# Kernel optimization log

Measured on AMD Instinct MI355X. Metric: run time of the kernel, lower is better.

## Reference

```python
import jax, jax.numpy as jnp
import numpy as np
import math

INPUT_DIM = 1024
DIM_K = 1024
DIM_V = 1024
B, N = 4, 2048

def setup_inputs() -> dict:
    key = jax.random.key(0)
    ks = jax.random.split(key, 7)
    s = 1.0 / math.sqrt(INPUT_DIM)
    return {
        'x':  jax.random.normal(ks[0], (B, N, INPUT_DIM), dtype=jnp.float32),
        'Wq': jax.random.uniform(ks[1], (DIM_K, INPUT_DIM), jnp.float32, -s, s),
        'bq': jax.random.uniform(ks[2], (DIM_K,), jnp.float32, -s, s),
        'Wk': jax.random.uniform(ks[3], (DIM_K, INPUT_DIM), jnp.float32, -s, s),
        'bk': jax.random.uniform(ks[4], (DIM_K,), jnp.float32, -s, s),
        'Wv': jax.random.uniform(ks[5], (DIM_V, INPUT_DIM), jnp.float32, -s, s),
        'bv': jax.random.uniform(ks[6], (DIM_V,), jnp.float32, -s, s),
    }

def reference(x, Wq, bq, Wk, bk, Wv, bv):
    norm_fact = 1.0 / math.sqrt(DIM_K)
    # torch Linear: y = x @ W.T + b
    Q = jnp.einsum('bnd,kd->bnk', x, Wq) + bq  # [B,N,dim_k]
    K = jnp.einsum('bnd,kd->bnk', x, Wk) + bk  # [B,N,dim_k]
    V = jnp.einsum('bnd,vd->bnv', x, Wv) + bv  # [B,N,dim_v]
    scores = jnp.einsum('bqk,bnk->bqn', Q, K)  # [B,N,N]
    # NOTE: original code applies softmax FIRST, then scales by norm_fact
    atten = jax.nn.softmax(scores, axis=-1) * norm_fact
    return jnp.einsum('bqn,bnv->bqv', atten, V)  # [B,N,dim_v]
```

## Files before the change

kernel.cpp:

```cpp
#include <hip/hip_runtime.h>


typedef _Float16 hfx8 __attribute__((ext_vector_type(8)));
typedef _Float16 hfx4 __attribute__((ext_vector_type(4)));
typedef float fx4 __attribute__((ext_vector_type(4)));

__device__ __forceinline__ void load_lds16(const void* g, void* l) {
    __builtin_amdgcn_global_load_lds(
        (const __attribute__((address_space(1))) void*)g,
        (__attribute__((address_space(3))) void*)l, 16, 0, 0);
}

template <int N> __device__ __forceinline__ void vmwait() {
    if constexpr (N == 8) asm volatile("s_waitcnt vmcnt(8)" ::: "memory");
    else if constexpr (N == 6) asm volatile("s_waitcnt vmcnt(6)" ::: "memory");
    else asm volatile("s_waitcnt vmcnt(0)" ::: "memory");
}

__device__ __forceinline__ void xcd_remap(int& x, int& y, int& z) {
    const int gx = gridDim.x, gy = gridDim.y;
    const int lin = blockIdx.x + gx * (blockIdx.y + gy * blockIdx.z);
    const int cpx = (gx * gy * gridDim.z) >> 3;
    const int w = (lin & 7) * cpx + (lin >> 3);
    x = w % gx;
    y = (w / gx) % gy;
    z = w / (gx * gy);
}

__global__ __launch_bounds__(256) void convx_kernel(
    const float4* __restrict__ in, _Float16* __restrict__ out)
{
    const int i = blockIdx.x * 256 + threadIdx.x;
    float4 v = in[i];
    hfx4 h;
    h[0] = (_Float16)v.x; h[1] = (_Float16)v.y;
    h[2] = (_Float16)v.z; h[3] = (_Float16)v.w;
    *(hfx4*)&out[(long)i * 4] = h;
}

__global__ __launch_bounds__(256) void convw3_kernel(
    const float4* __restrict__ w0, const float4* __restrict__ w1, const float4* __restrict__ w2,
    _Float16* __restrict__ o0, _Float16* __restrict__ o1, _Float16* __restrict__ o2)
{
    const int wsel = blockIdx.x >> 10;
    const float4* in = wsel == 0 ? w0 : (wsel == 1 ? w1 : w2);
    _Float16* out = wsel == 0 ? o0 : (wsel == 1 ? o1 : o2);
    const int i = (blockIdx.x & 1023) * 256 + threadIdx.x;
    float4 v = in[i];
    hfx4 h;
    h[0] = (_Float16)v.x; h[1] = (_Float16)v.y;
    h[2] = (_Float16)v.z; h[3] = (_Float16)v.w;
    *(hfx4*)&out[(long)i * 4] = h;
}

template <int OMODE>
__global__ __launch_bounds__(256, 2) void gemm2(
    const _Float16* __restrict__ A,
    const _Float16* __restrict__ Bq, const _Float16* __restrict__ Bk, const _Float16* __restrict__ Bv,
    const float* __restrict__ bq, const float* __restrict__ bk, const float* __restrict__ bv,
    float* __restrict__ outF, _Float16* __restrict__ oQ, _Float16* __restrict__ oK, _Float16* __restrict__ oV,
    int K, int lda, int ldb, int ldc, float alpha,
    long sAz, long sBz, long sCz)
{
    constexpr int BM = 128, BN = 128, BK = 64;
    constexpr int LPT = 8;

    __shared__ __attribute__((aligned(16))) _Float16 lds[2][(BM + BN) * BK];

    int bx, by, z;
    xcd_remap(bx, by, z);

    A += (long)z * sAz;
    const _Float16* B = (OMODE == 1) ? (z == 0 ? Bq : (z == 1 ? Bk : Bv))
                                     : Bq + (long)z * sBz;

    const int tid = threadIdx.x;
    const int lane = tid & 63;
    const int wv = tid >> 6;
    const int wr = wv >> 1, wc = wv & 1;
    const int lr = lane & 15, lk = lane >> 4;

    const long m0 = (long)by * BM;
    const long n0 = (long)bx * BN;

    fx4 acc[4][4] = {};

    auto STAGE = [&](int kt, int b) {
#pragma unroll
        for (int i = 0; i < LPT; ++i) {
            const int c = i * 256 + tid;
            if (i < 4) {
                const int row = c >> 3, slot = c & 7;
                load_lds16(A + (m0 + row) * (long)lda + kt + ((slot ^ (row & 7)) << 3),
                           &lds[b][c * 8]);
            } else {
                const int c2 = c - 1024;
                const int row = c2 >> 3, slot = c2 & 7;
                load_lds16(B + (n0 + row) * (long)ldb + kt + ((slot ^ (row & 7)) << 3),
                           &lds[b][BM * BK + c2 * 8]);
            }
        }
    };

    const int NT = K / BK;
    STAGE(0, 0);
    STAGE(BK, 1);
    vmwait<8>();
    __builtin_amdgcn_s_barrier();
    __builtin_amdgcn_sched_barrier(0);

    const int rA0 = wr * 64 + lr;
    const int rB0 = wc * 64 + lr;
    const int eA = (rA0 & 7) << 3;
    const int eB = (rB0 & 7) << 3;

    for (int t = 0; t < NT; ++t) {
        const _Float16* LA = &lds[t & 1][0];
        const _Float16* LB = LA + BM * BK;

        hfx8 bfr[4][2];
#pragma unroll
        for (int nf = 0; nf < 4; ++nf)
#pragma unroll
            for (int ks = 0; ks < 2; ++ks)
                bfr[nf][ks] = *(const hfx8*)&LB[(rB0 + nf * 16) * BK + ((ks * 32 + lk * 8) ^ eB)];

#pragma unroll
        for (int q = 0; q < 4; ++q) {
            hfx8 afr[2];
#pragma unroll
            for (int ks = 0; ks < 2; ++ks)
                afr[ks] = *(const hfx8*)&LA[(rA0 + q * 16) * BK + ((ks * 32 + lk * 8) ^ eA)];
            __builtin_amdgcn_s_setprio(1);
#pragma unroll
            for (int nf = 0; nf < 4; ++nf)
#pragma unroll
                for (int ks = 0; ks < 2; ++ks)
                    acc[q][nf] = __builtin_amdgcn_mfma_f32_16x16x32_f16(
                        afr[ks], bfr[nf][ks], acc[q][nf], 0, 0, 0);
            __builtin_amdgcn_s_setprio(0);
        }

        __builtin_amdgcn_s_barrier();
        if (t + 2 < NT) {
            STAGE((t + 2) * BK, t & 1);
            vmwait<8>();
        } else {
            vmwait<0>();
        }
        __builtin_amdgcn_s_barrier();
        __builtin_amdgcn_sched_barrier(0);
    }

#pragma unroll
    for (int mf = 0; mf < 4; ++mf) {
#pragma unroll
        for (int nf = 0; nf < 4; ++nf) {
            const long row0 = m0 + wr * 64 + mf * 16 + lk * 4;
            const long col = n0 + wc * 64 + nf * 16 + lr;
            if constexpr (OMODE == 0) {
                float* oz = outF + (long)z * sCz;
#pragma unroll
                for (int j = 0; j < 4; ++j)
                    oz[(row0 + j) * (long)ldc + col] = alpha * acc[mf][nf][j];
            } else {
                if (z == 0) {
                    const float bb = bq[col];
#pragma unroll
                    for (int j = 0; j < 4; ++j)
                        oQ[(row0 + j) * 1024 + col] = (_Float16)(acc[mf][nf][j] + bb);
                } else if (z == 1) {
                    const float bb = bk[col];
#pragma unroll
                    for (int j = 0; j < 4; ++j)
                        oK[(row0 + j) * 1024 + col] = (_Float16)(acc[mf][nf][j] + bb);
                } else {
                    const float bb = bv[col];
                    hfx4 pk;
#pragma unroll
                    for (int j = 0; j < 4; ++j) pk[j] = (_Float16)(acc[mf][nf][j] + bb);
                    *(hfx4*)&oV[((row0 >> 11) * 1024 + col) * 2048 + (row0 & 2047)] = pk;
                }
            }
        }
    }
}

__global__ __launch_bounds__(256) void softmax_kernel(float* __restrict__ S)
{
    const long row = blockIdx.x;
    float* r = S + row * 2048;
    const int t = threadIdx.x;

    float4 v0 = *(const float4*)&r[t * 4];
    float4 v1 = *(const float4*)&r[1024 + t * 4];
    float v[8] = {v0.x, v0.y, v0.z, v0.w, v1.x, v1.y, v1.z, v1.w};

    float mx = v[0];
#pragma unroll
    for (int j = 1; j < 8; ++j) mx = fmaxf(mx, v[j]);
#pragma unroll
    for (int o = 32; o; o >>= 1) mx = fmaxf(mx, __shfl_xor(mx, o, 64));

    __shared__ float redm[4];
    __shared__ float reds[4];
    const int w = t >> 6;
    if ((t & 63) == 0) redm[w] = mx;
    __syncthreads();
    mx = fmaxf(fmaxf(redm[0], redm[1]), fmaxf(redm[2], redm[3]));

    float e[8];
    float s = 0.f;
#pragma unroll
    for (int j = 0; j < 8; ++j) {
        e[j] = __expf(v[j] - mx);
        s += e[j];
    }
#pragma unroll
    for (int o = 32; o; o >>= 1) s += __shfl_xor(s, o, 64);
    if ((t & 63) == 0) reds[w] = s;
    __syncthreads();
    s = reds[0] + reds[1] + reds[2] + reds[3];

    const float inv = 1.0f / s;
    hfx4 p0, p1;
#pragma unroll
    for (int j = 0; j < 4; ++j) {
        p0[j] = (_Float16)(e[j] * inv);
        p1[j] = (_Float16)(e[4 + j] * inv);
    }
    _Float16* pr = (_Float16*)r;
    *(hfx4*)&pr[t * 4] = p0;
    *(hfx4*)&pr[1024 + t * 4] = p1;
}

extern "C" void kernel_launch(void* const* d_in, const int* in_sizes, int n_in,
                              void* d_out, int out_size, void* d_ws, size_t ws_size,
                              hipStream_t stream)
{
    const float* x  = (const float*)d_in[0];
    const float* Wq = (const float*)d_in[1];
    const float* bq = (const float*)d_in[2];
    const float* Wk = (const float*)d_in[3];
    const float* bk = (const float*)d_in[4];
    const float* Wv = (const float*)d_in[5];
    const float* bv = (const float*)d_in[6];
    float* out = (float*)d_out;

    _Float16* xs  = (_Float16*)d_ws;
    _Float16* Wqh = xs + 8192ull * 1024;
    _Float16* Wkh = Wqh + 1024ull * 1024;
    _Float16* Wvh = Wkh + 1024ull * 1024;
    _Float16* Qp  = Wvh + 1024ull * 1024;
    _Float16* Ks  = Qp + 8192ull * 1024;
    _Float16* Vt  = Ks + 8192ull * 1024;
    float* S      = (float*)(Vt + 4ull * 1024 * 2048);

    dim3 blk(256);

    convx_kernel<<<8192, blk, 0, stream>>>((const float4*)x, xs);
    convw3_kernel<<<3072, blk, 0, stream>>>(
        (const float4*)Wq, (const float4*)Wk, (const float4*)Wv, Wqh, Wkh, Wvh);

    gemm2<1><<<dim3(8, 64, 3), blk, 0, stream>>>(
        xs, Wqh, Wkh, Wvh, bq, bk, bv,
        nullptr, Qp, Ks, Vt,
        1024, 1024, 1024, 0, 1.0f, 0L, 0L, 0L);

    gemm2<0><<<dim3(16, 16, 4), blk, 0, stream>>>(
        Qp, Ks, nullptr, nullptr, nullptr, nullptr, nullptr,
        S, nullptr, nullptr, nullptr,
        1024, 1024, 1024, 2048, 1.0f,
        2097152L, 2097152L, 4194304L);

    softmax_kernel<<<2048 * 4, blk, 0, stream>>>(S);

    gemm2<0><<<dim3(8, 16, 4), blk, 0, stream>>>(
        (const _Float16*)S, Vt, nullptr, nullptr, nullptr, nullptr, nullptr,
        out, nullptr, nullptr, nullptr,
        2048, 4096, 2048, 1024, 0.03125f,
        8388608L, 2097152L, 2097152L);
}
```

Baseline: 178.5 us.

## Use 256x256-tile 8-wave GEMM with staged quarter prefetch for projections and QK^T

```diff
diff --git a/kernel.cpp b/kernel.cpp
--- a/kernel.cpp
+++ b/kernel.cpp
@@ -54,7 +54,7 @@
 }
 
 template <int OMODE>
-__global__ __launch_bounds__(256, 2) void gemm2(
+__global__ __launch_bounds__(512, 1) void gemm8p(
     const _Float16* __restrict__ A,
     const _Float16* __restrict__ Bq, const _Float16* __restrict__ Bk, const _Float16* __restrict__ Bv,
     const float* __restrict__ bq, const float* __restrict__ bk, const float* __restrict__ bv,
@@ -62,10 +62,8 @@
     int K, int lda, int ldb, int ldc, float alpha,
     long sAz, long sBz, long sCz)
 {
-    constexpr int BM = 128, BN = 128, BK = 64;
-    constexpr int LPT = 8;
-
-    __shared__ __attribute__((aligned(16))) _Float16 lds[2][(BM + BN) * BK];
+    constexpr int BK = 64;
+    __shared__ __attribute__((aligned(16))) _Float16 lds[2][32768];
 
     int bx, by, z;
     xcd_remap(bx, by, z);
@@ -73,6 +71,140 @@
     A += (long)z * sAz;
     const _Float16* B = (OMODE == 1) ? (z == 0 ? Bq : (z == 1 ? Bk : Bv))
                                      : Bq + (long)z * sBz;
+
+    const int tid = threadIdx.x;
+    const int lane = tid & 63;
+    const int wv = tid >> 6;
+    const int wr = wv >> 2, wc = wv & 3;
+    const int lr = lane & 15, lk = lane >> 4;
+
+    const long m0 = (long)by * 256;
+    const long n0 = (long)bx * 256;
+
+    fx4 acc[4][2][4] = {};
+
+    auto SH = [&](int kt, int b, int part, int h) {
+#pragma unroll
+        for (int i = 0; i < 2; ++i) {
+            const int g = i * 512 + tid;
+            const int row = h * 128 + (g >> 3);
+            const int slot = g & 7;
+            const _Float16* src = part ? (B + (n0 + row) * (long)ldb)
+                                       : (A + (m0 + row) * (long)lda);
+            load_lds16(src + kt + ((slot ^ (row & 7)) << 3),
+                       &lds[b][part * 16384 + row * 64 + slot * 8]);
+        }
+    };
+
+    const int NT = K / BK;
+    SH(0, 0, 1, 0); SH(0, 0, 1, 1); SH(0, 0, 0, 0); SH(0, 0, 0, 1);
+    SH(BK, 1, 1, 0); SH(BK, 1, 1, 1); SH(BK, 1, 0, 0);
+    vmwait<6>();
+    __builtin_amdgcn_s_barrier();
+
+    const int e = (lr & 7) << 3;
+
+    for (int t = 0; t < NT; ++t) {
+        const int b = t & 1;
+        const _Float16* LA = &lds[b][0];
+        const _Float16* LB = &lds[b][16384];
+
+        hfx8 bfr[4][2];
+#pragma unroll
+        for (int q = 0; q < 4; ++q) {
+            if (q == 0) {
+#pragma unroll
+                for (int nf = 0; nf < 4; ++nf)
+#pragma unroll
+                    for (int ks = 0; ks < 2; ++ks)
+                        bfr[nf][ks] = *(const hfx8*)&LB[(wc * 64 + nf * 16 + lr) * 64 + ((ks * 32 + lk * 8) ^ e)];
+            }
+            hfx8 afr[2][2];
+#pragma unroll
+            for (int j = 0; j < 2; ++j)
+#pragma unroll
+                for (int ks = 0; ks < 2; ++ks)
+                    afr[j][ks] = *(const hfx8*)&LA[(q * 64 + wr * 32 + j * 16 + lr) * 64 + ((ks * 32 + lk * 8) ^ e)];
+
+            if (q == 0)      { if (t + 1 < NT) SH((t + 1) * BK, b ^ 1, 0, 1); }
+            else if (q == 1) { if (t + 2 < NT) SH((t + 2) * BK, b, 1, 0); }
+            else if (q == 2) { if (t + 2 < NT) SH((t + 2) * BK, b, 1, 1); }
+            else             { if (t + 2 < NT) SH((t + 2) * BK, b, 0, 0); }
+
+            __builtin_amdgcn_s_barrier();
+            asm volatile("s_waitcnt lgkmcnt(0)" ::: "memory");
+            __builtin_amdgcn_sched_barrier(0);
+            __builtin_amdgcn_s_setprio(1);
+#pragma unroll
+            for (int j = 0; j < 2; ++j)
+#pragma unroll
+                for (int nf = 0; nf < 4; ++nf)
+#pragma unroll
+                    for (int ks = 0; ks < 2; ++ks)
+                        acc[q][j][nf] = __builtin_amdgcn_mfma_f32_16x16x32_f16(
+                            afr[j][ks], bfr[nf][ks], acc[q][j][nf], 0, 0, 0);
+            __builtin_amdgcn_s_setprio(0);
+            if (q == 3) {
+                if (t + 2 < NT) vmwait<6>();
+                else if (t + 1 < NT) vmwait<0>();
+            }
+            __builtin_amdgcn_s_barrier();
+        }
+    }
+
+#pragma unroll
+    for (int q = 0; q < 4; ++q) {
+#pragma unroll
+        for (int j = 0; j < 2; ++j) {
+#pragma unroll
+            for (int nf = 0; nf < 4; ++nf) {
+                const long row0 = m0 + q * 64 + wr * 32 + j * 16 + lk * 4;
+                const long col = n0 + wc * 64 + nf * 16 + lr;
+                if constexpr (OMODE == 0) {
+                    float* oz = outF + (long)z * sCz;
+#pragma unroll
+                    for (int jj = 0; jj < 4; ++jj)
+                        oz[(row0 + jj) * (long)ldc + col] = alpha * acc[q][j][nf][jj];
+                } else {
+                    if (z == 0) {
+                        const float bb = bq[col];
+#pragma unroll
+                        for (int jj = 0; jj < 4; ++jj)
+                            oQ[(row0 + jj) * 1024 + col] = (_Float16)(acc[q][j][nf][jj] + bb);
+                    } else if (z == 1) {
+                        const float bb = bk[col];
+#pragma unroll
+                        for (int jj = 0; jj < 4; ++jj)
+                            oK[(row0 + jj) * 1024 + col] = (_Float16)(acc[q][j][nf][jj] + bb);
+                    } else {
+                        const float bb = bv[col];
+                        hfx4 pk;
+#pragma unroll
+                        for (int jj = 0; jj < 4; ++jj) pk[jj] = (_Float16)(acc[q][j][nf][jj] + bb);
+                        *(hfx4*)&oV[((row0 >> 11) * 1024 + col) * 2048 + (row0 & 2047)] = pk;
+                    }
+                }
+            }
+        }
+    }
+}
+
+__global__ __launch_bounds__(256, 2) void gemm2(
+    const _Float16* __restrict__ A, const _Float16* __restrict__ B,
+    float* __restrict__ outF,
+    int K, int lda, int ldb, int ldc, float alpha,
+    long sAz, long sBz, long sCz)
+{
+    constexpr int BM = 128, BN = 128, BK = 64;
+    constexpr int LPT = 8;
+
+    __shared__ __attribute__((aligned(16))) _Float16 lds[2][(BM + BN) * BK];
+
+    int bx, by, z;
+    xcd_remap(bx, by, z);
+
+    A += (long)z * sAz;
+    B += (long)z * sBz;
 
     const int tid = threadIdx.x;
     const int lane = tid & 63;
@@ -158,30 +290,10 @@
         for (int nf = 0; nf < 4; ++nf) {
             const long row0 = m0 + wr * 64 + mf * 16 + lk * 4;
             const long col = n0 + wc * 64 + nf * 16 + lr;
-            if constexpr (OMODE == 0) {
-                float* oz = outF + (long)z * sCz;
-#pragma unroll
-                for (int j = 0; j < 4; ++j)
-                    oz[(row0 + j) * (long)ldc + col] = alpha * acc[mf][nf][j];
-            } else {
-                if (z == 0) {
-                    const float bb = bq[col];
-#pragma unroll
-                    for (int j = 0; j < 4; ++j)
-                        oQ[(row0 + j) * 1024 + col] = (_Float16)(acc[mf][nf][j] + bb);
-                } else if (z == 1) {
-                    const float bb = bk[col];
-#pragma unroll
-                    for (int j = 0; j < 4; ++j)
-                        oK[(row0 + j) * 1024 + col] = (_Float16)(acc[mf][nf][j] + bb);
-                } else {
-                    const float bb = bv[col];
-                    hfx4 pk;
-#pragma unroll
-                    for (int j = 0; j < 4; ++j) pk[j] = (_Float16)(acc[mf][nf][j] + bb);
-                    *(hfx4*)&oV[((row0 >> 11) * 1024 + col) * 2048 + (row0 & 2047)] = pk;
-                }
-            }
+            float* oz = outF + (long)z * sCz;
+#pragma unroll
+            for (int j = 0; j < 4; ++j)
+                oz[(row0 + j) * (long)ldc + col] = alpha * acc[mf][nf][j];
         }
     }
 }
@@ -262,12 +374,12 @@
     convw3_kernel<<<3072, blk, 0, stream>>>(
         (const float4*)Wq, (const float4*)Wk, (const float4*)Wv, Wqh, Wkh, Wvh);
 
-    gemm2<1><<<dim3(8, 64, 3), blk, 0, stream>>>(
+    gemm8p<1><<<dim3(4, 32, 3), 512, 0, stream>>>(
         xs, Wqh, Wkh, Wvh, bq, bk, bv,
         nullptr, Qp, Ks, Vt,
         1024, 1024, 1024, 0, 1.0f, 0L, 0L, 0L);
 
-    gemm2<0><<<dim3(16, 16, 4), blk, 0, stream>>>(
+    gemm8p<0><<<dim3(8, 8, 4), 512, 0, stream>>>(
         Qp, Ks, nullptr, nullptr, nullptr, nullptr, nullptr,
         S, nullptr, nullptr, nullptr,
         1024, 1024, 1024, 2048, 1.0f,
@@ -275,9 +387,8 @@
 
     softmax_kernel<<<2048 * 4, blk, 0, stream>>>(S);
 
-    gemm2<0><<<dim3(8, 16, 4), blk, 0, stream>>>(
-        (const _Float16*)S, Vt, nullptr, nullptr, nullptr, nullptr, nullptr,
-        out, nullptr, nullptr, nullptr,
+    gemm2<<<dim3(8, 16, 4), blk, 0, stream>>>(
+        (const _Float16*)S, Vt, out,
         2048, 4096, 2048, 1024, 0.03125f,
         8388608L, 2097152L, 2097152L);
 }
```

After: 185.7 us. 4.0% more time.

## Fold Q/K projections into a precomputed Wq^T·Wk matrix for attention scores

Applied to the files above, without the earlier changes.

```diff
diff --git a/kernel.cpp b/kernel.cpp
--- a/kernel.cpp
+++ b/kernel.cpp
@@ -13,7 +13,6 @@
 
 template <int N> __device__ __forceinline__ void vmwait() {
     if constexpr (N == 8) asm volatile("s_waitcnt vmcnt(8)" ::: "memory");
-    else if constexpr (N == 6) asm volatile("s_waitcnt vmcnt(6)" ::: "memory");
     else asm volatile("s_waitcnt vmcnt(0)" ::: "memory");
 }
 
@@ -27,38 +26,83 @@
     z = w / (gx * gy);
 }
 
-__global__ __launch_bounds__(256) void convx_kernel(
-    const float4* __restrict__ in, _Float16* __restrict__ out)
-{
-    const int i = blockIdx.x * 256 + threadIdx.x;
-    float4 v = in[i];
-    hfx4 h;
-    h[0] = (_Float16)v.x; h[1] = (_Float16)v.y;
-    h[2] = (_Float16)v.z; h[3] = (_Float16)v.w;
-    *(hfx4*)&out[(long)i * 4] = h;
-}
-
-__global__ __launch_bounds__(256) void convw3_kernel(
-    const float4* __restrict__ w0, const float4* __restrict__ w1, const float4* __restrict__ w2,
-    _Float16* __restrict__ o0, _Float16* __restrict__ o1, _Float16* __restrict__ o2)
-{
-    const int wsel = blockIdx.x >> 10;
-    const float4* in = wsel == 0 ? w0 : (wsel == 1 ? w1 : w2);
-    _Float16* out = wsel == 0 ? o0 : (wsel == 1 ? o1 : o2);
-    const int i = (blockIdx.x & 1023) * 256 + threadIdx.x;
-    float4 v = in[i];
-    hfx4 h;
-    h[0] = (_Float16)v.x; h[1] = (_Float16)v.y;
-    h[2] = (_Float16)v.z; h[3] = (_Float16)v.w;
-    *(hfx4*)&out[(long)i * 4] = h;
+__global__ __launch_bounds__(256) void transpose_w_kernel(
+    const float* __restrict__ Wq, const float* __restrict__ Wk,
+    _Float16* __restrict__ WqT, _Float16* __restrict__ WkT)
+{
+    const float* src = blockIdx.z ? Wk : Wq;
+    _Float16* dst = blockIdx.z ? WkT : WqT;
+    const int d0 = blockIdx.x * 64;
+    const int k0 = blockIdx.y * 64;
+    __shared__ float t[64][65];
+    const int tid = threadIdx.x;
+#pragma unroll
+    for (int i = 0; i < 4; ++i) {
+        const int r = i * 16 + (tid >> 4);
+        const int c = (tid & 15) * 4;
+        const float4 v = *(const float4*)&src[(long)(k0 + r) * 1024 + d0 + c];
+        t[r][c] = v.x; t[r][c + 1] = v.y; t[r][c + 2] = v.z; t[r][c + 3] = v.w;
+    }
+    __syncthreads();
+#pragma unroll
+    for (int i = 0; i < 2; ++i) {
+        const int d = i * 32 + (tid >> 3);
+        const int k = (tid & 7) * 8;
+        hfx8 h;
+#pragma unroll
+        for (int j = 0; j < 8; ++j) h[j] = (_Float16)t[k + j][d];
+        *(hfx8*)&dst[(long)(d0 + d) * 1024 + k0 + k] = h;
+    }
+}
+
+__global__ __launch_bounds__(256) void w2_kernel(
+    const float* __restrict__ bq, const float* __restrict__ Wk, float* __restrict__ w2)
+{
+    const int d = blockIdx.x * 256 + threadIdx.x;
+    float a = 0.f;
+    for (int k = 0; k < 1024; ++k)
+        a = fmaf(bq[k], Wk[(long)k * 1024 + d], a);
+    w2[d] = a;
+}
+
+__global__ __launch_bounds__(256) void conv_all_kernel(
+    const float4* __restrict__ x, _Float16* __restrict__ xs,
+    const float4* __restrict__ wv, _Float16* __restrict__ wvh,
+    const float* __restrict__ w2, float* __restrict__ v)
+{
+    const int b = blockIdx.x;
+    const int tid = threadIdx.x;
+    if (b < 8192) {
+        const long i = (long)b * 256 + tid;
+        const float4 xv = x[i];
+        hfx4 h;
+        h[0] = (_Float16)xv.x; h[1] = (_Float16)xv.y;
+        h[2] = (_Float16)xv.z; h[3] = (_Float16)xv.w;
+        *(hfx4*)&xs[i * 4] = h;
+        const float4 wval = *(const float4*)&w2[tid * 4];
+        float dot = xv.x * wval.x + xv.y * wval.y + xv.z * wval.z + xv.w * wval.w;
+#pragma unroll
+        for (int o = 32; o; o >>= 1) dot += __shfl_xor(dot, o, 64);
+        __shared__ float red[4];
+        if ((tid & 63) == 0) red[tid >> 6] = dot;
+        __syncthreads();
+        if (tid == 0) v[b] = red[0] + red[1] + red[2] + red[3];
+    } else {
+        const long i = (long)(b - 8192) * 256 + tid;
+        const float4 wv4 = wv[i];
+        hfx4 h;
+        h[0] = (_Float16)wv4.x; h[1] = (_Float16)wv4.y;
+        h[2] = (_Float16)wv4.z; h[3] = (_Float16)wv4.w;
+        *(hfx4*)&wvh[i * 4] = h;
+    }
 }
 
 template <int OMODE>
 __global__ __launch_bounds__(256, 2) void gemm2(
     const _Float16* __restrict__ A,
-    const _Float16* __restrict__ Bq, const _Float16* __restrict__ Bk, const _Float16* __restrict__ Bv,
-    const float* __restrict__ bq, const float* __restrict__ bk, const float* __restrict__ bv,
-    float* __restrict__ outF, _Float16* __restrict__ oQ, _Float16* __restrict__ oK, _Float16* __restrict__ oV,
+    const _Float16* __restrict__ B0, const _Float16* __restrict__ B1,
+    const float* __restrict__ bias, const float* __restrict__ cbias,
+    float* __restrict__ outF, _Float16* __restrict__ oH0, _Float16* __restrict__ oH1,
     int K, int lda, int ldb, int ldc, float alpha,
     long sAz, long sBz, long sCz)
 {
@@ -71,8 +115,7 @@
     xcd_remap(bx, by, z);
 
     A += (long)z * sAz;
-    const _Float16* B = (OMODE == 1) ? (z == 0 ? Bq : (z == 1 ? Bk : Bv))
-                                     : Bq + (long)z * sBz;
+    const _Float16* B = (OMODE == 1) ? (z == 0 ? B0 : B1) : B0 + (long)z * sBz;
 
     const int tid = threadIdx.x;
     const int lane = tid & 63;
@@ -160,26 +203,25 @@
             const long col = n0 + wc * 64 + nf * 16 + lr;
             if constexpr (OMODE == 0) {
                 float* oz = outF + (long)z * sCz;
+                const float cb = cbias ? cbias[(long)z * 2048 + col] : 0.0f;
 #pragma unroll
                 for (int j = 0; j < 4; ++j)
-                    oz[(row0 + j) * (long)ldc + col] = alpha * acc[mf][nf][j];
+                    oz[(row0 + j) * (long)ldc + col] = alpha * acc[mf][nf][j] + cb;
+            } else if constexpr (OMODE == 2) {
+#pragma unroll
+                for (int j = 0; j < 4; ++j)
+                    oH0[(row0 + j) * (long)ldc + col] = (_Float16)(alpha * acc[mf][nf][j]);
             } else {
                 if (z == 0) {
-                    const float bb = bq[col];
 #pragma unroll
                     for (int j = 0; j < 4; ++j)
-                        oQ[(row0 + j) * 1024 + col] = (_Float16)(acc[mf][nf][j] + bb);
-                } else if (z == 1) {
-                    const float bb = bk[col];
-#pragma unroll
-                    for (int j = 0; j < 4; ++j)
-                        oK[(row0 + j) * 1024 + col] = (_Float16)(acc[mf][nf][j] + bb);
+                        oH0[(row0 + j) * 1024 + col] = (_Float16)acc[mf][nf][j];
                 } else {
-                    const float bb = bv[col];
+                    const float bb = bias[col];
                     hfx4 pk;
 #pragma unroll
                     for (int j = 0; j < 4; ++j) pk[j] = (_Float16)(acc[mf][nf][j] + bb);
-                    *(hfx4*)&oV[((row0 >> 11) * 1024 + col) * 2048 + (row0 & 2047)] = pk;
+                    *(hfx4*)&oH1[((row0 >> 11) * 1024 + col) * 2048 + (row0 & 2047)] = pk;
                 }
             }
         }
@@ -246,38 +288,48 @@
     const float* Wv = (const float*)d_in[5];
     const float* bv = (const float*)d_in[6];
     float* out = (float*)d_out;
+    (void)bk;
 
     _Float16* xs  = (_Float16*)d_ws;
-    _Float16* Wqh = xs + 8192ull * 1024;
-    _Float16* Wkh = Wqh + 1024ull * 1024;
-    _Float16* Wvh = Wkh + 1024ull * 1024;
-    _Float16* Qp  = Wvh + 1024ull * 1024;
-    _Float16* Ks  = Qp + 8192ull * 1024;
-    _Float16* Vt  = Ks + 8192ull * 1024;
+    _Float16* Wvh = xs + 8192ull * 1024;
+    _Float16* WqT = Wvh + 1024ull * 1024;
+    _Float16* WkT = WqT + 1024ull * 1024;
+    _Float16* Mt  = WkT + 1024ull * 1024;
+    _Float16* Tt  = Mt + 1024ull * 1024;
+    _Float16* Vt  = Tt + 8192ull * 1024;
     float* S      = (float*)(Vt + 4ull * 1024 * 2048);
+    float* w2     = S + 4ull * 2048 * 2048;
+    float* v      = w2 + 1024;
 
     dim3 blk(256);
 
-    convx_kernel<<<8192, blk, 0, stream>>>((const float4*)x, xs);
-    convw3_kernel<<<3072, blk, 0, stream>>>(
-        (const float4*)Wq, (const float4*)Wk, (const float4*)Wv, Wqh, Wkh, Wvh);
-
-    gemm2<1><<<dim3(8, 64, 3), blk, 0, stream>>>(
-        xs, Wqh, Wkh, Wvh, bq, bk, bv,
-        nullptr, Qp, Ks, Vt,
+    transpose_w_kernel<<<dim3(16, 16, 2), blk, 0, stream>>>(Wq, Wk, WqT, WkT);
+    w2_kernel<<<4, blk, 0, stream>>>(bq, Wk, w2);
+
+    conv_all_kernel<<<9216, blk, 0, stream>>>(
+        (const float4*)x, xs, (const float4*)Wv, Wvh, w2, v);
+
+    gemm2<2><<<dim3(8, 8, 1), blk, 0, stream>>>(
+        WkT, WqT, nullptr, nullptr, nullptr,
+        nullptr, Mt, nullptr,
+        1024, 1024, 1024, 1024, 1.0f, 0L, 0L, 0L);
+
+    gemm2<1><<<dim3(8, 64, 2), blk, 0, stream>>>(
+        xs, Mt, Wvh, bv, nullptr,
+        nullptr, Tt, Vt,
         1024, 1024, 1024, 0, 1.0f, 0L, 0L, 0L);
 
     gemm2<0><<<dim3(16, 16, 4), blk, 0, stream>>>(
-        Qp, Ks, nullptr, nullptr, nullptr, nullptr, nullptr,
-        S, nullptr, nullptr, nullptr,
+        Tt, xs, nullptr, nullptr, v,
+        S, nullptr, nullptr,
         1024, 1024, 1024, 2048, 1.0f,
         2097152L, 2097152L, 4194304L);
 
     softmax_kernel<<<2048 * 4, blk, 0, stream>>>(S);
 
     gemm2<0><<<dim3(8, 16, 4), blk, 0, stream>>>(
-        (const _Float16*)S, Vt, nullptr, nullptr, nullptr, nullptr, nullptr,
-        out, nullptr, nullptr, nullptr,
+        (const _Float16*)S, Vt, nullptr, nullptr, nullptr,
+        out, nullptr, nullptr,
         2048, 4096, 2048, 1024, 0.03125f,
         8388608L, 2097152L, 2097152L);
 }
```

Result: slower. 203.3 us (+13.9%).
